# Kernel tuning notes

Hardware: AMD Instinct MI355X
Metric: run time of the kernel (lower is better)

## Reference

```python
import jax, jax.numpy as jnp
import numpy as np

EPS = 1e-5  # BatchNorm1d eps


def _glorot(key, shape):
    fan_in, fan_out = shape[0], shape[1]
    lim = float(np.sqrt(6.0 / (fan_in + fan_out)))
    return jax.random.uniform(key, shape, jnp.float32, -lim, lim)


def setup_inputs() -> dict:
    key = jax.random.key(0)
    ks = jax.random.split(key, 6)
    N, IN, H, OUT = 50000, 128, 64, 64
    E = 800000
    x = jax.random.normal(ks[0], (N, IN), jnp.float32)
    edge_index = jax.random.randint(ks[1], (2, E), 0, N, jnp.int64)
    return {
        "x": x,
        "edge_index": edge_index,
        "W1": _glorot(ks[2], (IN, H)),
        "b1": jnp.zeros((H,), jnp.float32),
        "gamma1": jnp.ones((H,), jnp.float32),
        "beta1": jnp.zeros((H,), jnp.float32),
        "W2": _glorot(ks[3], (H, OUT)),
        "b2": jnp.zeros((OUT,), jnp.float32),
        "gamma2": jnp.ones((OUT,), jnp.float32),
        "beta2": jnp.zeros((OUT,), jnp.float32),
    }


def _gcn_conv(x, W, b, src, dst, norm, n):
    # x' = D^{-1/2} (A + I) D^{-1/2} X W + b  (PyG GCNConv, edge_weight=None)
    h = x @ W                              # [N, F]
    msg = h[src] * norm[:, None]           # gather + scale, [E+N, F]
    out = jax.ops.segment_sum(msg, dst, num_segments=n)  # scatter-add
    return out + b


def _batch_norm(h, gamma, beta):
    # training-mode BN over node dim, biased variance (as torch uses for normalization)
    mean = h.mean(0)
    var = h.var(0)
    return (h - mean) * jax.lax.rsqrt(var + EPS) * gamma + beta


def reference(x, edge_index, W1, b1, gamma1, beta1, W2, b2, gamma2, beta2):
    n = x.shape[0]
    # add self loops
    loop = jnp.arange(n, dtype=edge_index.dtype)
    src = jnp.concatenate([edge_index[0], loop])
    dst = jnp.concatenate([edge_index[1], loop])
    # symmetric degree normalization (deg >= 1 thanks to self loops)
    deg = jax.ops.segment_sum(jnp.ones(src.shape[0], x.dtype), dst, num_segments=n)
    dinv = jax.lax.rsqrt(jnp.maximum(deg, 1e-12))
    norm = dinv[src] * dinv[dst]           # [E+N]

    # layer 1: GCNConv -> BN -> ReLU (dropout = identity in eval)
    h = _gcn_conv(x, W1, b1, src, dst, norm, n)
    h = jax.nn.relu(_batch_norm(h, gamma1, beta1))
    # layer 2: GCNConv -> BN (no activation on last layer)
    h = _gcn_conv(h, W2, b2, src, dst, norm, n)
    h = _batch_norm(h, gamma2, beta2)
    return h
```

## Files before the change

kernel.cpp:

```cpp
#include <hip/hip_runtime.h>
#include <hip/hip_fp16.h>
#include <math.h>

#define EPS 1e-5f
#define CAP 64

typedef float v4f __attribute__((ext_vector_type(4)));

__global__ void k_init(int* __restrict__ cnt, float* __restrict__ stats,
                       __half* __restrict__ Ylo, __half* __restrict__ Yhi,
                       unsigned short* __restrict__ csr, int N) {
    int i = blockIdx.x * blockDim.x + threadIdx.x;
    if (i < N) {
        cnt[i] = 0;
        int4* p = (int4*)(csr + (size_t)i * CAP);
#pragma unroll
        for (int k = 0; k < 8; ++k) p[k] = make_int4(-1, -1, -1, -1);
    }
    if (i < 256) stats[i] = 0.0f;
    if (i < 16) {
        ((int*)(Ylo + (size_t)N * 32))[i] = 0;
        ((int*)(Yhi + (size_t)N * 32))[i] = 0;
    }
}

__global__ void k_dinv(const int* __restrict__ cnt, float* __restrict__ dinv, int N) {
    int i = blockIdx.x * blockDim.x + threadIdx.x;
    if (i < N) dinv[i] = rsqrtf((float)(cnt[i] + 1));
    if (i == 0) dinv[N] = 0.0f;
}

__global__ __launch_bounds__(256) void k_gemm1_fill(const float* __restrict__ x,
                                                    const float* __restrict__ W1,
                                                    __half* __restrict__ Ylo,
                                                    __half* __restrict__ Yhi, int N,
                                                    const int* __restrict__ src,
                                                    const int* __restrict__ dst,
                                                    int* __restrict__ cnt,
                                                    unsigned short* __restrict__ csr,
                                                    int E, int G) {
    if ((int)blockIdx.x >= G) {
        int t = (blockIdx.x - G) * 256 + threadIdx.x;
        int stride = (gridDim.x - G) * 256;
        for (int e = t; e < E; e += stride) {
            int d = dst[e];
            int pos = atomicAdd(&cnt[d], 1);
            if (pos < CAP)
                __builtin_nontemporal_store((unsigned short)src[e], &csr[(size_t)d * CAP + pos]);
        }
        return;
    }
    __shared__ float w[128 * 64];
    __shared__ float xs[4][4][128];
    for (int i = threadIdx.x; i < 128 * 64; i += 256) w[i] = W1[i];
    __syncthreads();
    int lane = threadIdx.x & 63;
    int wave = threadIdx.x >> 6;
    int half = lane >> 5, l = lane & 31;
    __half* Yout = half ? Yhi : Ylo;
    int gwave = blockIdx.x * 4 + wave;
    int nw = G * 4;
    for (int r0 = gwave * 4; r0 < N; r0 += nw * 4) {
        int nr = min(4, N - r0);
        for (int j = 0; j < nr; ++j) {
            xs[wave][j][lane]      = x[(size_t)(r0 + j) * 128 + lane];
            xs[wave][j][64 + lane] = x[(size_t)(r0 + j) * 128 + 64 + lane];
        }
        float a0 = 0.f, a1 = 0.f, a2 = 0.f, a3 = 0.f;
#pragma unroll 8
        for (int k = 0; k < 128; ++k) {
            float wk = w[k * 64 + lane];
            a0 += xs[wave][0][k] * wk;
            a1 += xs[wave][1][k] * wk;
            a2 += xs[wave][2][k] * wk;
            a3 += xs[wave][3][k] * wk;
        }
        Yout[(size_t)(r0 + 0) * 32 + l] = __float2half(a0);
        if (nr > 1) Yout[(size_t)(r0 + 1) * 32 + l] = __float2half(a1);
        if (nr > 2) Yout[(size_t)(r0 + 2) * 32 + l] = __float2half(a2);
        if (nr > 3) Yout[(size_t)(r0 + 3) * 32 + l] = __float2half(a3);
    }
}

template <bool PRESCALED>
__global__ __launch_bounds__(256) void k_agg(const __half* __restrict__ Ylo,
                                             const __half* __restrict__ Yhi,
                                             const unsigned short* __restrict__ csr,
                                             const int* __restrict__ cnt,
                                             const float* __restrict__ dinv,
                                             float* __restrict__ H,
                                             float* __restrict__ stats, int N) {
    __shared__ float ssum[4][32], ssq[4][32];
    int half = blockIdx.x & 1;
    const __half* Y = half ? Yhi : Ylo;
    int lane = threadIdx.x & 63;
    int wave = threadIdx.x >> 6;
    int g = lane >> 3;
    int fl = lane & 7;
    int slot = (blockIdx.x >> 1) * 4 + wave;
    int nslots = (gridDim.x >> 1) * 4;
    float s0 = 0.f, s1 = 0.f, s2 = 0.f, s3 = 0.f;
    float q0 = 0.f, q1 = 0.f, q2 = 0.f, q3 = 0.f;
    union U8 { double d; __half2 h[2]; };
    for (int v = slot; v < N; v += nslots) {
        int c = min(cnt[v], CAP);
        float dv = dinv[v];
        int ent = (int)csr[(size_t)v * CAP + lane];
        float a0, a1, a2, a3;
        {
            U8 u; u.d = *(const double*)(Y + (size_t)v * 32 + fl * 4);
            float2 p0 = __half22float2(u.h[0]);
            float2 p1 = __half22float2(u.h[1]);
            float selfw = (g == 0) ? (PRESCALED ? 1.f : dv) : 0.f;
            a0 = selfw * p0.x; a1 = selfw * p0.y;
            a2 = selfw * p1.x; a3 = selfw * p1.y;
        }
        int nb = (c + 7) >> 3;
        for (int b = 0; b < nb; ++b) {
            int idx = __shfl(ent, b * 8 + g, 64);
            idx = min(idx, N);
            float de = PRESCALED ? 1.f : dinv[idx];
            U8 u; u.d = *(const double*)(Y + (size_t)idx * 32 + fl * 4);
            float2 p0 = __half22float2(u.h[0]);
            float2 p1 = __half22float2(u.h[1]);
            a0 += de * p0.x; a1 += de * p0.y;
            a2 += de * p1.x; a3 += de * p1.y;
        }
#pragma unroll
        for (int m = 8; m <= 32; m <<= 1) {
            a0 += __shfl_xor(a0, m, 64);
            a1 += __shfl_xor(a1, m, 64);
            a2 += __shfl_xor(a2, m, 64);
            a3 += __shfl_xor(a3, m, 64);
        }
        if (g == 0) {
            a0 *= dv; a1 *= dv; a2 *= dv; a3 *= dv;
            v4f hv = {a0, a1, a2, a3};
            __builtin_nontemporal_store(hv, (v4f*)(H + (size_t)v * 64 + half * 32 + fl * 4));
            s0 += a0; s1 += a1; s2 += a2; s3 += a3;
            q0 += a0 * a0; q1 += a1 * a1; q2 += a2 * a2; q3 += a3 * a3;
        }
    }
    if (g == 0) {
        ssum[wave][4 * fl + 0] = s0; ssum[wave][4 * fl + 1] = s1;
        ssum[wave][4 * fl + 2] = s2; ssum[wave][4 * fl + 3] = s3;
        ssq[wave][4 * fl + 0] = q0;  ssq[wave][4 * fl + 1] = q1;
        ssq[wave][4 * fl + 2] = q2;  ssq[wave][4 * fl + 3] = q3;
    }
    __syncthreads();
    if (threadIdx.x < 32) {
        float ts = ssum[0][threadIdx.x] + ssum[1][threadIdx.x] + ssum[2][threadIdx.x] + ssum[3][threadIdx.x];
        float tq = ssq[0][threadIdx.x] + ssq[1][threadIdx.x] + ssq[2][threadIdx.x] + ssq[3][threadIdx.x];
        atomicAdd(&stats[half * 32 + threadIdx.x], ts);
        atomicAdd(&stats[64 + half * 32 + threadIdx.x], tq);
    }
}

__global__ __launch_bounds__(256) void k_gemm2(const float* __restrict__ H1,
                                               const float* __restrict__ stats,
                                               const float* __restrict__ gamma,
                                               const float* __restrict__ beta,
                                               const float* __restrict__ W2,
                                               const float* __restrict__ dinv,
                                               __half* __restrict__ Ylo,
                                               __half* __restrict__ Yhi, int N) {
    __shared__ float w[64 * 64];
    __shared__ float xs[4][4][64];
    for (int i = threadIdx.x; i < 64 * 64; i += 256) w[i] = W2[i];
    int lane = threadIdx.x & 63;
    int wave = threadIdx.x >> 6;
    int half = lane >> 5, l = lane & 31;
    __half* Yout = half ? Yhi : Ylo;
    float mean = stats[lane] / (float)N;
    float var = stats[64 + lane] / (float)N - mean * mean;
    float rstd = rsqrtf(var + EPS);
    float g = gamma[lane], bt = beta[lane];
    __syncthreads();
    int gwave = blockIdx.x * 4 + wave;
    int nw = gridDim.x * 4;
    for (int r0 = gwave * 4; r0 < N; r0 += nw * 4) {
        int nr = min(4, N - r0);
        for (int j = 0; j < nr; ++j) {
            float v = H1[(size_t)(r0 + j) * 64 + lane];
            v = (v - mean) * rstd * g + bt;
            xs[wave][j][lane] = fmaxf(v, 0.f);
        }
        float a0 = 0.f, a1 = 0.f, a2 = 0.f, a3 = 0.f;
#pragma unroll 8
        for (int k = 0; k < 64; ++k) {
            float wk = w[k * 64 + lane];
            a0 += xs[wave][0][k] * wk;
            a1 += xs[wave][1][k] * wk;
            a2 += xs[wave][2][k] * wk;
            a3 += xs[wave][3][k] * wk;
        }
        Yout[(size_t)(r0 + 0) * 32 + l] = __float2half(a0 * dinv[r0]);
        if (nr > 1) Yout[(size_t)(r0 + 1) * 32 + l] = __float2half(a1 * dinv[r0 + 1]);
        if (nr > 2) Yout[(size_t)(r0 + 2) * 32 + l] = __float2half(a2 * dinv[r0 + 2]);
        if (nr > 3) Yout[(size_t)(r0 + 3) * 32 + l] = __float2half(a3 * dinv[r0 + 3]);
    }
}

__global__ void k_bnfinal(float* __restrict__ out, const float* __restrict__ stats,
                          const float* __restrict__ gamma, const float* __restrict__ beta,
                          int N) {
    int i = blockIdx.x * blockDim.x + threadIdx.x;
    int total = N * 64;
    if (i < total) {
        int f = i & 63;
        float mean = stats[f] / (float)N;
        float var = stats[64 + f] / (float)N - mean * mean;
        float rstd = rsqrtf(var + EPS);
        out[i] = (out[i] - mean) * rstd * gamma[f] + beta[f];
    }
}

extern "C" void kernel_launch(void* const* d_in, const int* in_sizes, int n_in,
                              void* d_out, int out_size, void* d_ws, size_t ws_size,
                              hipStream_t stream) {
    const float* x      = (const float*)d_in[0];
    const int*   ei     = (const int*)d_in[1];
    const float* W1     = (const float*)d_in[2];
    const float* gamma1 = (const float*)d_in[4];
    const float* beta1  = (const float*)d_in[5];
    const float* W2     = (const float*)d_in[6];
    const float* gamma2 = (const float*)d_in[8];
    const float* beta2  = (const float*)d_in[9];
    float* out = (float*)d_out;

    const int N = in_sizes[0] / 128;
    const int E = in_sizes[1] / 2;
    const int* src = ei;
    const int* dst = ei + E;

    char* ws = (char*)d_ws;
    int*   cnt   = (int*)  ws;
    float* stats = (float*)(ws + 0x40000);
    float* dinv  = (float*)(ws + 0x50000);
    __half* Ylo  = (__half*)(ws + 0x90000);
    __half* Yhi  = (__half*)(ws + 0x90000 + 0x320000);
    float* H1    = (float*)(ws + 0x90000 + 0x640000);
    unsigned short* csr = (unsigned short*)(ws + 0x90000 + 0x640000 + 0xC40000);

    const int B = (N + 255) / 256;
    const int total = N * 64;
    const int G = 768, F = 256;

    k_init<<<B, 256, 0, stream>>>(cnt, stats, Ylo, Yhi, csr, N);

    k_gemm1_fill<<<G + F, 256, 0, stream>>>(x, W1, Ylo, Yhi, N, src, dst, cnt, csr, E, G);
    k_dinv<<<B, 256, 0, stream>>>(cnt, dinv, N);
    k_agg<false><<<2048, 256, 0, stream>>>(Ylo, Yhi, csr, cnt, dinv, H1, stats, N);

    k_gemm2<<<1024, 256, 0, stream>>>(H1, stats, gamma1, beta1, W2, dinv, Ylo, Yhi, N);
    k_agg<true><<<2048, 256, 0, stream>>>(Ylo, Yhi, csr, cnt, dinv, out, stats + 128, N);
    k_bnfinal<<<(total + 255) / 256, 256, 0, stream>>>(out, stats + 128, gamma2, beta2, N);
}
```

Baseline: 268.3 us.

## Drop CSR prefill and dinv kernel; compute degree norm inline and prefetch rows

Removes the -1 fill of the CSR slot array and the separate dinv kernel. Invalid neighbor slots are now masked by comparing against the count, and the degree normalization is recomputed with rsqrtf from cnt wherever it is needed. The aggregation loop also prefetches the next node's count and CSR row to hide load latency. This cuts init memory traffic and one launch, at the cost of an extra dependent cnt gather per edge in the first aggregation. The workspace offsets for Y, H1 and csr are moved as well.

```diff
diff --git a/kernel.cpp b/kernel.cpp
--- a/kernel.cpp
+++ b/kernel.cpp
@@ -8,26 +8,14 @@
 typedef float v4f __attribute__((ext_vector_type(4)));
 
 __global__ void k_init(int* __restrict__ cnt, float* __restrict__ stats,
-                       __half* __restrict__ Ylo, __half* __restrict__ Yhi,
-                       unsigned short* __restrict__ csr, int N) {
+                       __half* __restrict__ Ylo, __half* __restrict__ Yhi, int N) {
     int i = blockIdx.x * blockDim.x + threadIdx.x;
-    if (i < N) {
-        cnt[i] = 0;
-        int4* p = (int4*)(csr + (size_t)i * CAP);
-#pragma unroll
-        for (int k = 0; k < 8; ++k) p[k] = make_int4(-1, -1, -1, -1);
-    }
+    if (i <= N) cnt[i] = 0;
     if (i < 256) stats[i] = 0.0f;
     if (i < 16) {
         ((int*)(Ylo + (size_t)N * 32))[i] = 0;
         ((int*)(Yhi + (size_t)N * 32))[i] = 0;
     }
-}
-
-__global__ void k_dinv(const int* __restrict__ cnt, float* __restrict__ dinv, int N) {
-    int i = blockIdx.x * blockDim.x + threadIdx.x;
-    if (i < N) dinv[i] = rsqrtf((float)(cnt[i] + 1));
-    if (i == 0) dinv[N] = 0.0f;
 }
 
 __global__ __launch_bounds__(256) void k_gemm1_fill(const float* __restrict__ x,
@@ -87,7 +75,6 @@
                                              const __half* __restrict__ Yhi,
                                              const unsigned short* __restrict__ csr,
                                              const int* __restrict__ cnt,
-                                             const float* __restrict__ dinv,
                                              float* __restrict__ H,
                                              float* __restrict__ stats, int N) {
     __shared__ float ssum[4][32], ssq[4][32];
@@ -102,10 +89,21 @@
     float s0 = 0.f, s1 = 0.f, s2 = 0.f, s3 = 0.f;
     float q0 = 0.f, q1 = 0.f, q2 = 0.f, q3 = 0.f;
     union U8 { double d; __half2 h[2]; };
+    int c_next = 0, ent_next = 0;
+    if (slot < N) {
+        c_next = cnt[slot];
+        ent_next = (int)csr[(size_t)slot * CAP + lane];
+    }
     for (int v = slot; v < N; v += nslots) {
-        int c = min(cnt[v], CAP);
-        float dv = dinv[v];
-        int ent = (int)csr[(size_t)v * CAP + lane];
+        int ct = c_next;
+        int ent = ent_next;
+        int vn = v + nslots;
+        if (vn < N) {
+            c_next = cnt[vn];
+            ent_next = (int)csr[(size_t)vn * CAP + lane];
+        }
+        int c = min(ct, CAP);
+        float dv = rsqrtf((float)(ct + 1));
         float a0, a1, a2, a3;
         {
             U8 u; u.d = *(const double*)(Y + (size_t)v * 32 + fl * 4);
@@ -117,9 +115,13 @@
         }
         int nb = (c + 7) >> 3;
         for (int b = 0; b < nb; ++b) {
-            int idx = __shfl(ent, b * 8 + g, 64);
-            idx = min(idx, N);
-            float de = PRESCALED ? 1.f : dinv[idx];
+            int sl = b * 8 + g;
+            bool valid = sl < c;
+            int idx = __shfl(ent, sl, 64);
+            idx &= 0xFFFF;
+            float de;
+            if (PRESCALED) de = valid ? 1.f : 0.f;
+            else           de = valid ? rsqrtf((float)(cnt[idx] + 1)) : 0.f;
             U8 u; u.d = *(const double*)(Y + (size_t)idx * 32 + fl * 4);
             float2 p0 = __half22float2(u.h[0]);
             float2 p1 = __half22float2(u.h[1]);
@@ -161,7 +163,7 @@
                                                const float* __restrict__ gamma,
                                                const float* __restrict__ beta,
                                                const float* __restrict__ W2,
-                                               const float* __restrict__ dinv,
+                                               const int* __restrict__ cnt,
                                                __half* __restrict__ Ylo,
                                                __half* __restrict__ Yhi, int N) {
     __shared__ float w[64 * 64];
@@ -194,10 +196,11 @@
             a2 += xs[wave][2][k] * wk;
             a3 += xs[wave][3][k] * wk;
         }
-        Yout[(size_t)(r0 + 0) * 32 + l] = __float2half(a0 * dinv[r0]);
-        if (nr > 1) Yout[(size_t)(r0 + 1) * 32 + l] = __float2half(a1 * dinv[r0 + 1]);
-        if (nr > 2) Yout[(size_t)(r0 + 2) * 32 + l] = __float2half(a2 * dinv[r0 + 2]);
-        if (nr > 3) Yout[(size_t)(r0 + 3) * 32 + l] = __float2half(a3 * dinv[r0 + 3]);
+        float d0 = rsqrtf((float)(cnt[r0] + 1));
+        Yout[(size_t)(r0 + 0) * 32 + l] = __float2half(a0 * d0);
+        if (nr > 1) Yout[(size_t)(r0 + 1) * 32 + l] = __float2half(a1 * rsqrtf((float)(cnt[r0 + 1] + 1)));
+        if (nr > 2) Yout[(size_t)(r0 + 2) * 32 + l] = __float2half(a2 * rsqrtf((float)(cnt[r0 + 2] + 1)));
+        if (nr > 3) Yout[(size_t)(r0 + 3) * 32 + l] = __float2half(a3 * rsqrtf((float)(cnt[r0 + 3] + 1)));
     }
 }
 
@@ -236,23 +239,21 @@
     char* ws = (char*)d_ws;
     int*   cnt   = (int*)  ws;
     float* stats = (float*)(ws + 0x40000);
-    float* dinv  = (float*)(ws + 0x50000);
     __half* Ylo  = (__half*)(ws + 0x90000);
-    __half* Yhi  = (__half*)(ws + 0x90000 + 0x320000);
-    float* H1    = (float*)(ws + 0x90000 + 0x640000);
-    unsigned short* csr = (unsigned short*)(ws + 0x90000 + 0x640000 + 0xC40000);
-
-    const int B = (N + 255) / 256;
+    __half* Yhi  = (__half*)(ws + 0x90000 + 0x500000);
+    float* H1    = (float*)(ws + 0x90000 + 0xA00000);
+    unsigned short* csr = (unsigned short*)(ws + 0x90000 + 0xA00000 + 0xC40000);
+
+    const int B = (N + 256) / 256;
     const int total = N * 64;
     const int G = 768, F = 256;
 
-    k_init<<<B, 256, 0, stream>>>(cnt, stats, Ylo, Yhi, csr, N);
+    k_init<<<B, 256, 0, stream>>>(cnt, stats, Ylo, Yhi, N);
 
     k_gemm1_fill<<<G + F, 256, 0, stream>>>(x, W1, Ylo, Yhi, N, src, dst, cnt, csr, E, G);
-    k_dinv<<<B, 256, 0, stream>>>(cnt, dinv, N);
-    k_agg<false><<<2048, 256, 0, stream>>>(Ylo, Yhi, csr, cnt, dinv, H1, stats, N);
-
-    k_gemm2<<<1024, 256, 0, stream>>>(H1, stats, gamma1, beta1, W2, dinv, Ylo, Yhi, N);
-    k_agg<true><<<2048, 256, 0, stream>>>(Ylo, Yhi, csr, cnt, dinv, out, stats + 128, N);
+    k_agg<false><<<2048, 256, 0, stream>>>(Ylo, Yhi, csr, cnt, H1, stats, N);
+
+    k_gemm2<<<1024, 256, 0, stream>>>(H1, stats, gamma1, beta1, W2, cnt, Ylo, Yhi, N);
+    k_agg<true><<<2048, 256, 0, stream>>>(Ylo, Yhi, csr, cnt, out, stats + 128, N);
     k_bnfinal<<<(total + 255) / 256, 256, 0, stream>>>(out, stats + 128, gamma2, beta2, N);
 }
```

Result: no change. 270.5 us (+0.8%).
